# Kernel tuning notes

Measured on AMD Instinct MI355X. Metric: run time of the kernel, lower is better.

## Reference

```python
import jax, jax.numpy as jnp
import numpy as np

N_NODES = 65536
N_EDGES = 524288
GRAPH_SIZE = 512  # equal-size graphs -> batch = arange(N)//512
N_GRAPHS = N_NODES // GRAPH_SIZE
IN_DIM, HID, OUT_DIM, HEADS = 64, 64, 128, 4


def setup_inputs() -> dict:
    key = jax.random.key(0)
    ks = jax.random.split(key, 24)
    s = 0.1  # init scale
    # within-graph random edges
    g = jax.random.randint(ks[0], (N_EDGES,), 0, N_GRAPHS)
    off = jax.random.randint(ks[1], (2, N_EDGES), 0, GRAPH_SIZE)
    edge_index = (g[None, :] * GRAPH_SIZE + off).astype(jnp.int32)
    batch = (jnp.arange(N_NODES) // GRAPH_SIZE).astype(jnp.int32)
    rn = lambda k, sh: jax.random.normal(k, sh, jnp.float32) * s
    return {
        'x': jax.random.normal(ks[2], (N_NODES, IN_DIM), jnp.float32),
        'edge_index': edge_index, 'batch': batch,
        'W1': rn(ks[3], (IN_DIM, HEADS * HID)), 'a1s': rn(ks[4], (HEADS, HID)),
        'a1d': rn(ks[5], (HEADS, HID)), 'b1': jnp.zeros((HEADS * HID,), jnp.float32),
        'W2': rn(ks[6], (HEADS * HID, HEADS * HID)), 'a2s': rn(ks[7], (HEADS, HID)),
        'a2d': rn(ks[8], (HEADS, HID)), 'b2': jnp.zeros((HEADS * HID,), jnp.float32),
        'W3': rn(ks[9], (HEADS * HID, OUT_DIM)), 'a3s': rn(ks[10], (1, OUT_DIM)),
        'a3d': rn(ks[11], (1, OUT_DIM)), 'b3': jnp.zeros((OUT_DIM,), jnp.float32),
        'g1': jnp.ones((HEADS * HID,), jnp.float32), 'be1': jnp.zeros((HEADS * HID,), jnp.float32),
        'g2': jnp.ones((HEADS * HID,), jnp.float32), 'be2': jnp.zeros((HEADS * HID,), jnp.float32),
        'Wr': rn(ks[12], (IN_DIM, OUT_DIM)), 'br': jnp.zeros((OUT_DIM,), jnp.float32),
        'Wq': rn(ks[13], (OUT_DIM, OUT_DIM)), 'Wk': rn(ks[14], (OUT_DIM, OUT_DIM)),
        'Wv': rn(ks[15], (OUT_DIM, OUT_DIM)), 'Wo': rn(ks[16], (OUT_DIM, OUT_DIM)),
        'bo': jnp.zeros((OUT_DIM,), jnp.float32),
    }


def _gat(x, src, dst, W, a_s, a_d, b, heads, out_ch):
    N = x.shape[0]
    h = (x @ W).reshape(N, heads, out_ch)          # [N,H,C]
    e_s = (h * a_s).sum(-1)                        # [N,H]
    e_d = (h * a_d).sum(-1)
    e = jax.nn.leaky_relu(e_s[src] + e_d[dst], 0.2)  # [E,H]
    m = jax.ops.segment_max(e, dst, num_segments=N)
    p = jnp.exp(e - m[dst])
    z = jax.ops.segment_sum(p, dst, num_segments=N)
    alpha = p / (z[dst] + 1e-16)
    out = jax.ops.segment_sum(alpha[:, :, None] * h[src], dst, num_segments=N)
    return out.reshape(N, heads * out_ch) + b


def _ln(x, g, b):
    mu = x.mean(-1, keepdims=True)
    v = ((x - mu) ** 2).mean(-1, keepdims=True)
    return (x - mu) * jax.lax.rsqrt(v + 1e-5) * g + b


def _mha(x, Wq, Wk, Wv, Wo, bo, heads):
    B, n, D = x.shape
    hd = D // heads
    q = (x @ Wq).reshape(B, n, heads, hd)
    k = (x @ Wk).reshape(B, n, heads, hd)
    v = (x @ Wv).reshape(B, n, heads, hd)
    energy = jnp.einsum('bqhd,bkhd->bhqk', q, k)
    att = jax.nn.softmax(energy / jnp.sqrt(jnp.float32(D)), axis=-1)
    out = jnp.einsum('bhqk,bkhd->bqhd', att, v).reshape(B, n, D)
    return out @ Wo + bo


def reference(x, edge_index, batch, W1, a1s, a1d, b1, W2, a2s, a2d, b2,
              W3, a3s, a3d, b3, g1, be1, g2, be2, Wr, br, Wq, Wk, Wv, Wo, bo):
    N = x.shape[0]
    loops = jnp.arange(N, dtype=edge_index.dtype)
    src = jnp.concatenate([edge_index[0], loops])  # PyG add_self_loops default
    dst = jnp.concatenate([edge_index[1], loops])
    h = jax.nn.elu(_gat(x, src, dst, W1, a1s, a1d, b1, HEADS, HID))
    h = _ln(h, g1, be1)
    h = jax.nn.elu(_gat(h, src, dst, W2, a2s, a2d, b2, HEADS, HID))
    h = _ln(h, g2, be2)
    h = _gat(h, src, dst, W3, a3s, a3d, b3, 1, OUT_DIM)
    h = h + (x @ Wr + br)
    # equal-size graphs: per-graph self-attention via batched reshape
    hg = h.reshape(N_GRAPHS, GRAPH_SIZE, OUT_DIM)
    hg = _mha(hg, Wq, Wk, Wv, Wo, bo, 4)
    return hg.reshape(N, OUT_DIM)
```

## Files before the change

### kernel.cpp

```cpp
#include <hip/hip_runtime.h>
#include <math.h>

#define N_NODES 65536
#define NUM_EDGES 524288
#define E_TOT   (NUM_EDGES + N_NODES)
#define GSZ 512

typedef _Float16 f16x8 __attribute__((ext_vector_type(8)));
typedef _Float16 f16x4 __attribute__((ext_vector_type(4)));
typedef _Float16 f16x2 __attribute__((ext_vector_type(2)));
typedef float    f32x16 __attribute__((ext_vector_type(16)));

__global__ void k_zero_int(int* __restrict__ p, int n) {
  int i = blockIdx.x * blockDim.x + threadIdx.x;
  if (i < n) p[i] = 0;
}

__global__ void k_hist(const int* __restrict__ ei, int* __restrict__ cnt) {
  int e = blockIdx.x * blockDim.x + threadIdx.x;
  if (e >= E_TOT) return;
  int dst = (e < NUM_EDGES) ? ei[NUM_EDGES + e] : (e - NUM_EDGES);
  atomicAdd(&cnt[dst], 1);
}

__global__ void k_scan1(const int* __restrict__ cnt, int* __restrict__ offs,
                        int* __restrict__ sums) {
  __shared__ int s[256];
  int t = threadIdx.x;
  int i = blockIdx.x * 256 + t;
  int v = cnt[i];
  s[t] = v;
  for (int o = 1; o < 256; o <<= 1) {
    __syncthreads();
    int x = (t >= o) ? s[t - o] : 0;
    __syncthreads();
    s[t] += x;
  }
  offs[i] = s[t] - v;
  if (t == 255) sums[blockIdx.x] = s[t];
}

__global__ void k_scan2(int* __restrict__ sums) {
  __shared__ int s[256];
  int t = threadIdx.x;
  int v = sums[t];
  s[t] = v;
  for (int o = 1; o < 256; o <<= 1) {
    __syncthreads();
    int x = (t >= o) ? s[t - o] : 0;
    __syncthreads();
    s[t] += x;
  }
  sums[t] = s[t] - v;
}

__global__ void k_scan3(int* __restrict__ offs, const int* __restrict__ sums,
                        int* __restrict__ cur) {
  int i = blockIdx.x * 256 + threadIdx.x;
  int v = offs[i] + sums[blockIdx.x];
  offs[i] = v;
  cur[i] = v;
  if (i == 0) offs[N_NODES] = E_TOT;
}

__global__ void k_fill(const int* __restrict__ ei, int* __restrict__ cur,
                       int* __restrict__ ssrc) {
  int e = blockIdx.x * blockDim.x + threadIdx.x;
  if (e >= E_TOT) return;
  int src, dst;
  if (e < NUM_EDGES) { src = ei[e]; dst = ei[NUM_EDGES + e]; }
  else               { src = e - NUM_EDGES; dst = src; }
  int pos = atomicAdd(&cur[dst], 1);
  ssrc[pos] = src;
}

__device__ __forceinline__ f16x8 cvt8(float4 a, float4 b) {
  f16x8 h;
  h[0] = (_Float16)a.x; h[1] = (_Float16)a.y;
  h[2] = (_Float16)a.z; h[3] = (_Float16)a.w;
  h[4] = (_Float16)b.x; h[5] = (_Float16)b.y;
  h[6] = (_Float16)b.z; h[7] = (_Float16)b.w;
  return h;
}

#define LDH 40
template <typename TA, typename TC>
__global__ __launch_bounds__(256) void k_gemm(
    const TA* __restrict__ A, const float* __restrict__ B,
    const float* __restrict__ bias, TC* __restrict__ C,
    int M, int N, int K, float cscale) {
  __shared__ __align__(16) _Float16 As[128][LDH];
  __shared__ __align__(16) _Float16 Bs[128][LDH];
  const int t = threadIdx.x;
  const int l = t & 63, w = t >> 6;
  const int m0 = blockIdx.x * 128, n0 = blockIdx.y * 128;
  const int wm = (w >> 1) * 64, wn = (w & 1) * 64;
  const int lm = l & 31, kq = l >> 5;

  f32x16 acc00 = {}, acc01 = {}, acc10 = {}, acc11 = {};

  const int ra = t >> 1, ka = (t & 1) << 4;
  const int nb = (t & 31) << 2, kb = (t >> 5) << 2;

  for (int k0 = 0; k0 < K; k0 += 32) {
    f16x8 a_lo, a_hi;
    if constexpr (sizeof(TA) == 4) {
      const float* ap = (const float*)&A[(size_t)(m0 + ra) * K + k0 + ka];
      float4 av0 = *(const float4*)ap;
      float4 av1 = *(const float4*)(ap + 4);
      float4 av2 = *(const float4*)(ap + 8);
      float4 av3 = *(const float4*)(ap + 12);
      a_lo = cvt8(av0, av1);
      a_hi = cvt8(av2, av3);
    } else {
      const _Float16* ap = (const _Float16*)&A[(size_t)(m0 + ra) * K + k0 + ka];
      a_lo = *(const f16x8*)ap;
      a_hi = *(const f16x8*)(ap + 8);
    }
    const float* bp = &B[(size_t)(k0 + kb) * N + n0 + nb];
    float4 bv0 = *(const float4*)bp;
    float4 bv1 = *(const float4*)(bp + N);
    float4 bv2 = *(const float4*)(bp + 2 * N);
    float4 bv3 = *(const float4*)(bp + 3 * N);
    __syncthreads();
    *(f16x8*)&As[ra][ka]     = a_lo;
    *(f16x8*)&As[ra][ka + 8] = a_hi;
    f16x4 g;
    g[0] = (_Float16)bv0.x; g[1] = (_Float16)bv1.x;
    g[2] = (_Float16)bv2.x; g[3] = (_Float16)bv3.x;
    *(f16x4*)&Bs[nb + 0][kb] = g;
    g[0] = (_Float16)bv0.y; g[1] = (_Float16)bv1.y;
    g[2] = (_Float16)bv2.y; g[3] = (_Float16)bv3.y;
    *(f16x4*)&Bs[nb + 1][kb] = g;
    g[0] = (_Float16)bv0.z; g[1] = (_Float16)bv1.z;
    g[2] = (_Float16)bv2.z; g[3] = (_Float16)bv3.z;
    *(f16x4*)&Bs[nb + 2][kb] = g;
    g[0] = (_Float16)bv0.w; g[1] = (_Float16)bv1.w;
    g[2] = (_Float16)bv2.w; g[3] = (_Float16)bv3.w;
    *(f16x4*)&Bs[nb + 3][kb] = g;
    __syncthreads();
#pragma unroll
    for (int ks = 0; ks < 2; ++ks) {
      f16x8 a0 = *(const f16x8*)&As[wm + lm][ks * 16 + kq * 8];
      f16x8 a1 = *(const f16x8*)&As[wm + 32 + lm][ks * 16 + kq * 8];
      f16x8 b0 = *(const f16x8*)&Bs[wn + lm][ks * 16 + kq * 8];
      f16x8 b1 = *(const f16x8*)&Bs[wn + 32 + lm][ks * 16 + kq * 8];
      acc00 = __builtin_amdgcn_mfma_f32_32x32x16_f16(a0, b0, acc00, 0, 0, 0);
      acc01 = __builtin_amdgcn_mfma_f32_32x32x16_f16(a0, b1, acc01, 0, 0, 0);
      acc10 = __builtin_amdgcn_mfma_f32_32x32x16_f16(a1, b0, acc10, 0, 0, 0);
      acc11 = __builtin_amdgcn_mfma_f32_32x32x16_f16(a1, b1, acc11, 0, 0, 0);
    }
  }

  const int cn = n0 + wn + lm;
  float b0v = 0.f, b1v = 0.f;
  if (bias) { b0v = bias[cn]; b1v = bias[cn + 32]; }
  const int rb = 4 * (l >> 5);
#pragma unroll
  for (int r = 0; r < 16; ++r) {
    int row = m0 + wm + (r & 3) + 8 * (r >> 2) + rb;
    C[(size_t)row * N + cn]             = (TC)((acc00[r] + b0v) * cscale);
    C[(size_t)row * N + cn + 32]        = (TC)((acc01[r] + b1v) * cscale);
    C[(size_t)(row + 32) * N + cn]      = (TC)((acc10[r] + b0v) * cscale);
    C[(size_t)(row + 32) * N + cn + 32] = (TC)((acc11[r] + b1v) * cscale);
  }
}

__global__ void k_scores(const _Float16* __restrict__ h, const float* __restrict__ as_,
                         const float* __restrict__ ad_, float* __restrict__ es,
                         float* __restrict__ ed, int H, int C) {
  int t = blockIdx.x * blockDim.x + threadIdx.x;
  if (t >= N_NODES * H) return;
  int hd = t % H;
  const _Float16* hp = h + (size_t)t * C;
  const float* ap = as_ + hd * C;
  const float* dp = ad_ + hd * C;
  float s = 0.f, d = 0.f;
  for (int c = 0; c < C; c += 8) {
    f16x8 hv = *(const f16x8*)&hp[c];
    float4 a0 = *(const float4*)&ap[c];
    float4 a1 = *(const float4*)&ap[c + 4];
    float4 d0 = *(const float4*)&dp[c];
    float4 d1 = *(const float4*)&dp[c + 4];
    float h0 = (float)hv[0], h1 = (float)hv[1], h2 = (float)hv[2], h3 = (float)hv[3];
    float h4 = (float)hv[4], h5 = (float)hv[5], h6 = (float)hv[6], h7 = (float)hv[7];
    s += h0 * a0.x + h1 * a0.y + h2 * a0.z + h3 * a0.w;
    s += h4 * a1.x + h5 * a1.y + h6 * a1.z + h7 * a1.w;
    d += h0 * d0.x + h1 * d0.y + h2 * d0.z + h3 * d0.w;
    d += h4 * d1.x + h5 * d1.y + h6 * d1.z + h7 * d1.w;
  }
  es[t] = s; ed[t] = d;
}

__device__ __forceinline__ float lrelu02(float e) { return e >= 0.f ? e : 0.2f * e; }

__global__ __launch_bounds__(256) void k_agg256(
    const _Float16* __restrict__ h, const float* __restrict__ es,
    const float* __restrict__ ed, const int* __restrict__ offs,
    const int* __restrict__ ssrc, const float* __restrict__ bias,
    const float* __restrict__ lng, const float* __restrict__ lnb,
    _Float16* __restrict__ out) {
  int lane = threadIdx.x & 63;
  int bid = blockIdx.x;
  int swz = (bid & 7) * ((int)gridDim.x >> 3) + (bid >> 3);
  int n = swz * 4 + (threadIdx.x >> 6);
  int head = lane >> 4;
  int o0 = offs[n], deg = offs[n + 1] - o0;
  float4 edv = *(const float4*)&ed[n * 4];
  float edh = (head & 2) ? ((head & 1) ? edv.w : edv.z)
                         : ((head & 1) ? edv.y : edv.x);
  float z = 0.f, a0 = 0.f, a1 = 0.f, a2 = 0.f, a3 = 0.f;
  int c0 = lane * 4;
  int j = 0;
  for (; j + 2 <= deg; j += 2) {
    int s0 = ssrc[o0 + j], s1 = ssrc[o0 + j + 1];
    float p0 = __expf(fminf(lrelu02(es[s0 * 4 + head] + edh), 80.f));
    float p1 = __expf(fminf(lrelu02(es[s1 * 4 + head] + edh), 80.f));
    f16x4 h0 = *(const f16x4*)&h[(size_t)s0 * 256 + c0];
    f16x4 h1 = *(const f16x4*)&h[(size_t)s1 * 256 + c0];
    z += p0 + p1;
    a0 += p0 * (float)h0[0] + p1 * (float)h1[0];
    a1 += p0 * (float)h0[1] + p1 * (float)h1[1];
    a2 += p0 * (float)h0[2] + p1 * (float)h1[2];
    a3 += p0 * (float)h0[3] + p1 * (float)h1[3];
  }
  if (j < deg) {
    int s0 = ssrc[o0 + j];
    float p0 = __expf(fminf(lrelu02(es[s0 * 4 + head] + edh), 80.f));
    f16x4 h0 = *(const f16x4*)&h[(size_t)s0 * 256 + c0];
    z += p0;
    a0 += p0 * (float)h0[0]; a1 += p0 * (float)h0[1];
    a2 += p0 * (float)h0[2]; a3 += p0 * (float)h0[3];
  }
  float inv = 1.f / (z + 1e-16f);
  float4 bv = *(const float4*)&bias[c0];
  float v0 = a0 * inv + bv.x; v0 = v0 > 0.f ? v0 : __expf(v0) - 1.f;
  float v1 = a1 * inv + bv.y; v1 = v1 > 0.f ? v1 : __expf(v1) - 1.f;
  float v2 = a2 * inv + bv.z; v2 = v2 > 0.f ? v2 : __expf(v2) - 1.f;
  float v3 = a3 * inv + bv.w; v3 = v3 > 0.f ? v3 : __expf(v3) - 1.f;
  float sum = v0 + v1 + v2 + v3;
#pragma unroll
  for (int o = 1; o < 64; o <<= 1) sum += __shfl_xor(sum, o);
  float mean = sum * (1.f / 256.f);
  float d0 = v0 - mean, d1 = v1 - mean, d2 = v2 - mean, d3 = v3 - mean;
  float sq = d0 * d0 + d1 * d1 + d2 * d2 + d3 * d3;
#pragma unroll
  for (int o = 1; o < 64; o <<= 1) sq += __shfl_xor(sq, o);
  float rs = rsqrtf(sq * (1.f / 256.f) + 1e-5f);
  float4 gv = *(const float4*)&lng[c0];
  float4 ev2 = *(const float4*)&lnb[c0];
  f16x4 o4;
  o4[0] = (_Float16)(d0 * rs * gv.x + ev2.x);
  o4[1] = (_Float16)(d1 * rs * gv.y + ev2.y);
  o4[2] = (_Float16)(d2 * rs * gv.z + ev2.z);
  o4[3] = (_Float16)(d3 * rs * gv.w + ev2.w);
  *(f16x4*)&out[(size_t)n * 256 + c0] = o4;
}

__global__ __launch_bounds__(256) void k_agg128(
    const _Float16* __restrict__ h, const float* __restrict__ es,
    const float* __restrict__ ed, const int* __restrict__ offs,
    const int* __restrict__ ssrc, const float* __restrict__ bias,
    float* __restrict__ io) {
  int lane = threadIdx.x & 63;
  int bid = blockIdx.x;
  int swz = (bid & 7) * ((int)gridDim.x >> 3) + (bid >> 3);
  int n = swz * 4 + (threadIdx.x >> 6);
  int o0 = offs[n], deg = offs[n + 1] - o0;
  float edv = ed[n];
  float z = 0.f, a0 = 0.f, a1 = 0.f;
  int c0 = lane * 2;
  int j = 0;
  for (; j + 2 <= deg; j += 2) {
    int s0 = ssrc[o0 + j], s1 = ssrc[o0 + j + 1];
    float p0 = __expf(fminf(lrelu02(es[s0] + edv), 80.f));
    float p1 = __expf(fminf(lrelu02(es[s1] + edv), 80.f));
    f16x2 h0 = *(const f16x2*)&h[(size_t)s0 * 128 + c0];
    f16x2 h1 = *(const f16x2*)&h[(size_t)s1 * 128 + c0];
    z += p0 + p1;
    a0 += p0 * (float)h0[0] + p1 * (float)h1[0];
    a1 += p0 * (float)h0[1] + p1 * (float)h1[1];
  }
  if (j < deg) {
    int s0 = ssrc[o0 + j];
    float p0 = __expf(fminf(lrelu02(es[s0] + edv), 80.f));
    f16x2 h0 = *(const f16x2*)&h[(size_t)s0 * 128 + c0];
    z += p0;
    a0 += p0 * (float)h0[0]; a1 += p0 * (float)h0[1];
  }
  float inv = 1.f / (z + 1e-16f);
  float2 r = *(const float2*)&io[(size_t)n * 128 + c0];
  float2 o2;
  o2.x = a0 * inv + bias[c0]     + r.x;
  o2.y = a1 * inv + bias[c0 + 1] + r.y;
  *(float2*)&io[(size_t)n * 128 + c0] = o2;
}

__global__ __launch_bounds__(512) void k_attn(
    const _Float16* __restrict__ Q, const _Float16* __restrict__ K,
    const _Float16* __restrict__ V, _Float16* __restrict__ O) {
  __shared__ __align__(16) _Float16 Ks[64][40];
  __shared__ __align__(16) _Float16 VsT[32][72];
  const int g = blockIdx.x >> 2, hd = blockIdx.x & 3;
  const int t = threadIdx.x;
  const int l = t & 63, w = t >> 6;
  const int h = l >> 5, l31 = l & 31;
  const size_t base = (size_t)g * (GSZ * 128) + hd * 32;

  f16x8 qf[2][2];
#pragma unroll
  for (int j = 0; j < 2; ++j)
#pragma unroll
    for (int ks = 0; ks < 2; ++ks)
      qf[j][ks] = *(const f16x8*)&Q[base + (size_t)(w * 64 + j * 32 + l31) * 128 + ks * 16 + 8 * h];

  f32x16 o0 = {}, o1 = {};
  float la0 = 0.f, la1 = 0.f, m0 = -1e30f, m1 = -1e30f;

  const int kr = t >> 3, dc = (t & 7) * 4;
  for (int kt = 0; kt < GSZ; kt += 64) {
    f16x4 kg = *(const f16x4*)&K[base + (size_t)(kt + kr) * 128 + dc];
    f16x4 vg = *(const f16x4*)&V[base + (size_t)(kt + kr) * 128 + dc];
    __syncthreads();
    *(f16x4*)&Ks[kr][dc] = kg;
    VsT[dc + 0][kr] = vg[0];
    VsT[dc + 1][kr] = vg[1];
    VsT[dc + 2][kr] = vg[2];
    VsT[dc + 3][kr] = vg[3];
    __syncthreads();

#pragma unroll
    for (int s2 = 0; s2 < 2; ++s2) {
      f16x8 ka0 = *(const f16x8*)&Ks[s2 * 32 + l31][8 * h];
      f16x8 ka1 = *(const f16x8*)&Ks[s2 * 32 + l31][16 + 8 * h];
      f16x8 va0 = *(const f16x8*)&VsT[l31][s2 * 32 + 8 * h];
      f16x8 va1 = *(const f16x8*)&VsT[l31][s2 * 32 + 16 + 8 * h];
#pragma unroll
      for (int j = 0; j < 2; ++j) {
        f32x16 s = {};
        s = __builtin_amdgcn_mfma_f32_32x32x16_f16(ka0, qf[j][0], s, 0, 0, 0);
        s = __builtin_amdgcn_mfma_f32_32x32x16_f16(ka1, qf[j][1], s, 0, 0, 0);
        float tm = s[0];
#pragma unroll
        for (int r = 1; r < 16; ++r) tm = fmaxf(tm, s[r]);
        tm = fmaxf(tm, __shfl_xor(tm, 32));
        float* mj = j ? &m1 : &m0;
        float* lj = j ? &la1 : &la0;
        f32x16* oj = j ? &o1 : &o0;
        if (tm > *mj + 10.f) {
          float sc = exp2f(*mj - tm);
          *lj *= sc;
#pragma unroll
          for (int r = 0; r < 16; ++r) (*oj)[r] *= sc;
          *mj = tm;
        }
        float p[16]; float ls = 0.f;
#pragma unroll
        for (int r = 0; r < 16; ++r) { p[r] = exp2f(s[r] - *mj); ls += p[r]; }
        *lj += ls;
#pragma unroll
        for (int kk = 0; kk < 2; ++kk) {
          const int rb = kk * 8;
          unsigned a01 = __builtin_bit_cast(unsigned, __builtin_amdgcn_cvt_pkrtz(p[rb + 0], p[rb + 1]));
          unsigned a23 = __builtin_bit_cast(unsigned, __builtin_amdgcn_cvt_pkrtz(p[rb + 2], p[rb + 3]));
          unsigned b01 = __builtin_bit_cast(unsigned, __builtin_amdgcn_cvt_pkrtz(p[rb + 4], p[rb + 5]));
          unsigned b23 = __builtin_bit_cast(unsigned, __builtin_amdgcn_cvt_pkrtz(p[rb + 6], p[rb + 7]));
          unsigned sa01 = (unsigned)__shfl_xor((int)a01, 32);
          unsigned sa23 = (unsigned)__shfl_xor((int)a23, 32);
          unsigned sb01 = (unsigned)__shfl_xor((int)b01, 32);
          unsigned sb23 = (unsigned)__shfl_xor((int)b23, 32);
          union { unsigned u[4]; f16x8 v; } pb;
          pb.u[0] = h ? sb01 : a01;
          pb.u[1] = h ? sb23 : a23;
          pb.u[2] = h ? b01 : sa01;
          pb.u[3] = h ? b23 : sa23;
          *oj = __builtin_amdgcn_mfma_f32_32x32x16_f16(kk ? va1 : va0, pb.v, *oj, 0, 0, 0);
        }
      }
    }
  }

  la0 += __shfl_xor(la0, 32);
  la1 += __shfl_xor(la1, 32);
  const float i0 = 1.f / la0, i1 = 1.f / la1;
#pragma unroll
  for (int r = 0; r < 16; ++r) {
    int dv = (r & 3) + 8 * (r >> 2) + 4 * h;
    O[base + (size_t)(w * 64 + l31) * 128 + dv]      = (_Float16)(o0[r] * i0);
    O[base + (size_t)(w * 64 + 32 + l31) * 128 + dv] = (_Float16)(o1[r] * i1);
  }
}

extern "C" void kernel_launch(void* const* d_in, const int* in_sizes, int n_in,
                              void* d_out, int out_size, void* d_ws, size_t ws_size,
                              hipStream_t stream) {
  (void)in_sizes; (void)n_in; (void)out_size; (void)ws_size;
  const float* x   = (const float*)d_in[0];
  const int*   ei  = (const int*)d_in[1];
  const float* W1  = (const float*)d_in[3];
  const float* a1s = (const float*)d_in[4];
  const float* a1d = (const float*)d_in[5];
  const float* b1  = (const float*)d_in[6];
  const float* W2  = (const float*)d_in[7];
  const float* a2s = (const float*)d_in[8];
  const float* a2d = (const float*)d_in[9];
  const float* b2  = (const float*)d_in[10];
  const float* W3  = (const float*)d_in[11];
  const float* a3s = (const float*)d_in[12];
  const float* a3d = (const float*)d_in[13];
  const float* b3  = (const float*)d_in[14];
  const float* g1  = (const float*)d_in[15];
  const float* be1 = (const float*)d_in[16];
  const float* g2  = (const float*)d_in[17];
  const float* be2 = (const float*)d_in[18];
  const float* Wr  = (const float*)d_in[19];
  const float* br  = (const float*)d_in[20];
  const float* Wq  = (const float*)d_in[21];
  const float* Wk  = (const float*)d_in[22];
  const float* Wv  = (const float*)d_in[23];
  const float* Wo  = (const float*)d_in[24];
  const float* bo  = (const float*)d_in[25];
  float* out = (float*)d_out;

  _Float16* Hbuf = (_Float16*)d_ws;
  _Float16* Abuf = Hbuf + (size_t)N_NODES * 256;
  float* esb = (float*)(Abuf + (size_t)N_NODES * 256);
  float* edb = esb + (size_t)N_NODES * 4;
  int* offs = (int*)(edb + (size_t)N_NODES * 4);
  int* cur  = offs + N_NODES + 4;
  int* ssrc = cur + N_NODES;
  int* sums = ssrc + E_TOT;

  dim3 blk(256), blk512(512);
  k_zero_int<<<256, blk, 0, stream>>>(cur, N_NODES);
  k_hist<<<(E_TOT + 255) / 256, blk, 0, stream>>>(ei, cur);
  k_scan1<<<256, blk, 0, stream>>>(cur, offs, sums);
  k_scan2<<<1, blk, 0, stream>>>(sums);
  k_scan3<<<256, blk, 0, stream>>>(offs, sums, cur);
  k_fill<<<(E_TOT + 255) / 256, blk, 0, stream>>>(ei, cur, ssrc);

  dim3 gN128(512, 1), gN256(512, 2);
  const float qsc = 0.0883883476483184f * 1.44269504088896f;

  k_gemm<float, float><<<gN128, blk, 0, stream>>>(x, Wr, br, out, N_NODES, 128, 64, 1.f);

  k_gemm<float, _Float16><<<gN256, blk, 0, stream>>>(x, W1, nullptr, Hbuf, N_NODES, 256, 64, 1.f);
  k_scores<<<N_NODES * 4 / 256, blk, 0, stream>>>(Hbuf, a1s, a1d, esb, edb, 4, 64);
  k_agg256<<<N_NODES / 4, blk, 0, stream>>>(Hbuf, esb, edb, offs, ssrc, b1, g1, be1, Abuf);
  k_gemm<_Float16, _Float16><<<gN256, blk, 0, stream>>>(Abuf, W2, nullptr, Hbuf, N_NODES, 256, 256, 1.f);
  k_scores<<<N_NODES * 4 / 256, blk, 0, stream>>>(Hbuf, a2s, a2d, esb, edb, 4, 64);
  k_agg256<<<N_NODES / 4, blk, 0, stream>>>(Hbuf, esb, edb, offs, ssrc, b2, g2, be2, Abuf);
  k_gemm<_Float16, _Float16><<<gN128, blk, 0, stream>>>(Abuf, W3, nullptr, Hbuf, N_NODES, 128, 256, 1.f);
  k_scores<<<N_NODES / 256, blk, 0, stream>>>(Hbuf, a3s, a3d, esb, edb, 1, 128);
  k_agg128<<<N_NODES / 4, blk, 0, stream>>>(Hbuf, esb, edb, offs, ssrc, b3, out);

  _Float16* Qb  = Abuf;
  _Float16* Kb  = Abuf + (size_t)N_NODES * 128;
  _Float16* Vb  = Hbuf;
  _Float16* AOb = Hbuf + (size_t)N_NODES * 128;
  k_gemm<float, _Float16><<<gN128, blk, 0, stream>>>(out, Wq, nullptr, Qb, N_NODES, 128, 128, qsc);
  k_gemm<float, _Float16><<<gN128, blk, 0, stream>>>(out, Wk, nullptr, Kb, N_NODES, 128, 128, 1.f);
  k_gemm<float, _Float16><<<gN128, blk, 0, stream>>>(out, Wv, nullptr, Vb, N_NODES, 128, 128, 1.f);
  k_attn<<<512, blk512, 0, stream>>>(Qb, Kb, Vb, AOb);
  k_gemm<_Float16, float><<<gN128, blk, 0, stream>>>(AOb, Wo, bo, out, N_NODES, 128, 128, 1.f);
}
```

Before: 534.9 us.

## Fuse QKV projections into one GEMM and double-buffer attention K/V tiles

Concatenates Wq, Wk and Wv into one 128x384 weight matrix so a single GEMM produces Q, K and V in an interleaved buffer, with the softmax scale applied only to the Q column block. This reads the activation input once instead of three times and saves two launches. The attention kernel now uses 256-thread blocks, each covering half of a graph's queries, and double-buffers the K/V shared-memory tiles so the next tile's global load overlaps the MFMA work. The trade-off is a small weight-concat kernel on every call, strided 384-wide reads of K/V, and K/V tiles loaded twice per head (once per query half).

```diff
diff --git a/kernel.cpp b/kernel.cpp
--- a/kernel.cpp
+++ b/kernel.cpp
@@ -74,6 +74,17 @@
   ssrc[pos] = src;
 }
 
+__global__ void k_catw(const float* __restrict__ Wq, const float* __restrict__ Wk,
+                       const float* __restrict__ Wv, float* __restrict__ Wcat) {
+  int i = blockIdx.x * 256 + threadIdx.x;
+  if (i >= 128 * 384) return;
+  int k = i / 384, j = i - k * 384;
+  float v = (j < 128) ? Wq[k * 128 + j]
+          : (j < 256) ? Wk[k * 128 + j - 128]
+                      : Wv[k * 128 + j - 256];
+  Wcat[i] = v;
+}
+
 __device__ __forceinline__ f16x8 cvt8(float4 a, float4 b) {
   f16x8 h;
   h[0] = (_Float16)a.x; h[1] = (_Float16)a.y;
@@ -88,7 +99,7 @@
 __global__ __launch_bounds__(256) void k_gemm(
     const TA* __restrict__ A, const float* __restrict__ B,
     const float* __restrict__ bias, TC* __restrict__ C,
-    int M, int N, int K, float cscale) {
+    int M, int N, int K, float cscale, int sy) {
   __shared__ __align__(16) _Float16 As[128][LDH];
   __shared__ __align__(16) _Float16 Bs[128][LDH];
   const int t = threadIdx.x;
@@ -96,6 +107,7 @@
   const int m0 = blockIdx.x * 128, n0 = blockIdx.y * 128;
   const int wm = (w >> 1) * 64, wn = (w & 1) * 64;
   const int lm = l & 31, kq = l >> 5;
+  const float cs = (blockIdx.y == sy) ? cscale : 1.f;
 
   f32x16 acc00 = {}, acc01 = {}, acc10 = {}, acc11 = {};
 
@@ -159,10 +171,10 @@
 #pragma unroll
   for (int r = 0; r < 16; ++r) {
     int row = m0 + wm + (r & 3) + 8 * (r >> 2) + rb;
-    C[(size_t)row * N + cn]             = (TC)((acc00[r] + b0v) * cscale);
-    C[(size_t)row * N + cn + 32]        = (TC)((acc01[r] + b1v) * cscale);
-    C[(size_t)(row + 32) * N + cn]      = (TC)((acc10[r] + b0v) * cscale);
-    C[(size_t)(row + 32) * N + cn + 32] = (TC)((acc11[r] + b1v) * cscale);
+    C[(size_t)row * N + cn]             = (TC)((acc00[r] + b0v) * cs);
+    C[(size_t)row * N + cn + 32]        = (TC)((acc01[r] + b1v) * cs);
+    C[(size_t)(row + 32) * N + cn]      = (TC)((acc10[r] + b0v) * cs);
+    C[(size_t)(row + 32) * N + cn + 32] = (TC)((acc11[r] + b1v) * cs);
   }
 }
 
@@ -296,53 +308,65 @@
   *(float2*)&io[(size_t)n * 128 + c0] = o2;
 }
 
-__global__ __launch_bounds__(512) void k_attn(
-    const _Float16* __restrict__ Q, const _Float16* __restrict__ K,
-    const _Float16* __restrict__ V, _Float16* __restrict__ O) {
-  __shared__ __align__(16) _Float16 Ks[64][40];
-  __shared__ __align__(16) _Float16 VsT[32][72];
-  const int g = blockIdx.x >> 2, hd = blockIdx.x & 3;
+__global__ __launch_bounds__(256) void k_attn(
+    const _Float16* __restrict__ QKV, _Float16* __restrict__ O) {
+  __shared__ __align__(16) _Float16 Ks[2][64][40];
+  __shared__ __align__(16) _Float16 VsT[2][32][72];
+  const int bid = blockIdx.x;
+  const int g = bid >> 3, hd = (bid >> 1) & 3, qh = bid & 1;
   const int t = threadIdx.x;
   const int l = t & 63, w = t >> 6;
   const int h = l >> 5, l31 = l & 31;
-  const size_t base = (size_t)g * (GSZ * 128) + hd * 32;
+  const size_t nbase = (size_t)g * GSZ;
+  const _Float16* Qp = QKV + hd * 32;
+  const _Float16* Kp = QKV + 128 + hd * 32;
+  const _Float16* Vp = QKV + 256 + hd * 32;
 
   f16x8 qf[2][2];
 #pragma unroll
   for (int j = 0; j < 2; ++j)
 #pragma unroll
     for (int ks = 0; ks < 2; ++ks)
-      qf[j][ks] = *(const f16x8*)&Q[base + (size_t)(w * 64 + j * 32 + l31) * 128 + ks * 16 + 8 * h];
+      qf[j][ks] = *(const f16x8*)&Qp[(nbase + qh * 256 + w * 64 + j * 32 + l31) * 384 + ks * 16 + 8 * h];
 
   f32x16 o0 = {}, o1 = {};
   float la0 = 0.f, la1 = 0.f, m0 = -1e30f, m1 = -1e30f;
 
-  const int kr = t >> 3, dc = (t & 7) * 4;
+  const int kr = t >> 2, dcc = (t & 3) * 8;
+  {
+    f16x8 kg = *(const f16x8*)&Kp[(nbase + kr) * 384 + dcc];
+    f16x8 vg = *(const f16x8*)&Vp[(nbase + kr) * 384 + dcc];
+    *(f16x8*)&Ks[0][kr][dcc] = kg;
+#pragma unroll
+    for (int i = 0; i < 8; ++i) VsT[0][dcc + i][kr] = vg[i];
+  }
+  __syncthreads();
+
   for (int kt = 0; kt < GSZ; kt += 64) {
-    f16x4 kg = *(const f16x4*)&K[base + (size_t)(kt + kr) * 128 + dc];
-    f16x4 vg = *(const f16x4*)&V[base + (size_t)(kt + kr) * 128 + dc];
-    __syncthreads();
-    *(f16x4*)&Ks[kr][dc] = kg;
-    VsT[dc + 0][kr] = vg[0];
-    VsT[dc + 1][kr] = vg[1];
-    VsT[dc + 2][kr] = vg[2];
-    VsT[dc + 3][kr] = vg[3];
-    __syncthreads();
-
+    const int cur = (kt >> 6) & 1;
+    const bool more = (kt + 64) < GSZ;
+    f16x8 kn, vn;
+    if (more) {
+      kn = *(const f16x8*)&Kp[(nbase + kt + 64 + kr) * 384 + dcc];
+      vn = *(const f16x8*)&Vp[(nbase + kt + 64 + kr) * 384 + dcc];
+    }
 #pragma unroll
     for (int s2 = 0; s2 < 2; ++s2) {
-      f16x8 ka0 = *(const f16x8*)&Ks[s2 * 32 + l31][8 * h];
-      f16x8 ka1 = *(const f16x8*)&Ks[s2 * 32 + l31][16 + 8 * h];
-      f16x8 va0 = *(const f16x8*)&VsT[l31][s2 * 32 + 8 * h];
-      f16x8 va1 = *(const f16x8*)&VsT[l31][s2 * 32 + 16 + 8 * h];
+      f16x8 ka0 = *(const f16x8*)&Ks[cur][s2 * 32 + l31][8 * h];
+      f16x8 ka1 = *(const f16x8*)&Ks[cur][s2 * 32 + l31][16 + 8 * h];
+      f16x8 va0 = *(const f16x8*)&VsT[cur][l31][s2 * 32 + 8 * h];
+      f16x8 va1 = *(const f16x8*)&VsT[cur][l31][s2 * 32 + 16 + 8 * h];
 #pragma unroll
       for (int j = 0; j < 2; ++j) {
         f32x16 s = {};
         s = __builtin_amdgcn_mfma_f32_32x32x16_f16(ka0, qf[j][0], s, 0, 0, 0);
         s = __builtin_amdgcn_mfma_f32_32x32x16_f16(ka1, qf[j][1], s, 0, 0, 0);
-        float tm = s[0];
-#pragma unroll
-        for (int r = 1; r < 16; ++r) tm = fmaxf(tm, s[r]);
+        float t0 = fmaxf(fmaxf(s[0], s[1]), s[2]);
+        float t1 = fmaxf(fmaxf(s[3], s[4]), s[5]);
+        float t2 = fmaxf(fmaxf(s[6], s[7]), s[8]);
+        float t3 = fmaxf(fmaxf(s[9], s[10]), s[11]);
+        float t4 = fmaxf(fmaxf(s[12], s[13]), s[14]);
+        float tm = fmaxf(fmaxf(fmaxf(t0, t1), fmaxf(t2, t3)), fmaxf(t4, s[15]));
         tm = fmaxf(tm, __shfl_xor(tm, 32));
         float* mj = j ? &m1 : &m0;
         float* lj = j ? &la1 : &la0;
@@ -378,6 +402,12 @@
         }
       }
     }
+    if (more) {
+      *(f16x8*)&Ks[cur ^ 1][kr][dcc] = kn;
+#pragma unroll
+      for (int i = 0; i < 8; ++i) VsT[cur ^ 1][dcc + i][kr] = vn[i];
+    }
+    __syncthreads();
   }
 
   la0 += __shfl_xor(la0, 32);
@@ -386,8 +416,8 @@
 #pragma unroll
   for (int r = 0; r < 16; ++r) {
     int dv = (r & 3) + 8 * (r >> 2) + 4 * h;
-    O[base + (size_t)(w * 64 + l31) * 128 + dv]      = (_Float16)(o0[r] * i0);
-    O[base + (size_t)(w * 64 + 32 + l31) * 128 + dv] = (_Float16)(o1[r] * i1);
+    O[(nbase + qh * 256 + w * 64 + l31) * 128 + hd * 32 + dv]      = (_Float16)(o0[r] * i0);
+    O[(nbase + qh * 256 + w * 64 + 32 + l31) * 128 + hd * 32 + dv] = (_Float16)(o1[r] * i1);
   }
 }
 
@@ -424,43 +454,41 @@
 
   _Float16* Hbuf = (_Float16*)d_ws;
   _Float16* Abuf = Hbuf + (size_t)N_NODES * 256;
-  float* esb = (float*)(Abuf + (size_t)N_NODES * 256);
+  _Float16* QKVb = Abuf + (size_t)N_NODES * 256;
+  _Float16* AOb  = QKVb + (size_t)N_NODES * 384;
+  float* esb = (float*)(AOb + (size_t)N_NODES * 128);
   float* edb = esb + (size_t)N_NODES * 4;
-  int* offs = (int*)(edb + (size_t)N_NODES * 4);
+  float* Wcat = edb + (size_t)N_NODES * 4;
+  int* offs = (int*)(Wcat + 128 * 384);
   int* cur  = offs + N_NODES + 4;
   int* ssrc = cur + N_NODES;
   int* sums = ssrc + E_TOT;
 
-  dim3 blk(256), blk512(512);
+  dim3 blk(256);
   k_zero_int<<<256, blk, 0, stream>>>(cur, N_NODES);
   k_hist<<<(E_TOT + 255) / 256, blk, 0, stream>>>(ei, cur);
   k_scan1<<<256, blk, 0, stream>>>(cur, offs, sums);
   k_scan2<<<1, blk, 0, stream>>>(sums);
   k_scan3<<<256, blk, 0, stream>>>(offs, sums, cur);
   k_fill<<<(E_TOT + 255) / 256, blk, 0, stream>>>(ei, cur, ssrc);
-
-  dim3 gN128(512, 1), gN256(512, 2);
+  k_catw<<<192, blk, 0, stream>>>(Wq, Wk, Wv, Wcat);
+
+  dim3 gN128(512, 1), gN256(512, 2), gN384(512, 3);
   const float qsc = 0.0883883476483184f * 1.44269504088896f;
 
-  k_gemm<float, float><<<gN128, blk, 0, stream>>>(x, Wr, br, out, N_NODES, 128, 64, 1.f);
-
-  k_gemm<float, _Float16><<<gN256, blk, 0, stream>>>(x, W1, nullptr, Hbuf, N_NODES, 256, 64, 1.f);
+  k_gemm<float, float><<<gN128, blk, 0, stream>>>(x, Wr, br, out, N_NODES, 128, 64, 1.f, -1);
+
+  k_gemm<float, _Float16><<<gN256, blk, 0, stream>>>(x, W1, nullptr, Hbuf, N_NODES, 256, 64, 1.f, -1);
   k_scores<<<N_NODES * 4 / 256, blk, 0, stream>>>(Hbuf, a1s, a1d, esb, edb, 4, 64);
   k_agg256<<<N_NODES / 4, blk, 0, stream>>>(Hbuf, esb, edb, offs, ssrc, b1, g1, be1, Abuf);
-  k_gemm<_Float16, _Float16><<<gN256, blk, 0, stream>>>(Abuf, W2, nullptr, Hbuf, N_NODES, 256, 256, 1.f);
+  k_gemm<_Float16, _Float16><<<gN256, blk, 0, stream>>>(Abuf, W2, nullptr, Hbuf, N_NODES, 256, 256, 1.f, -1);
   k_scores<<<N_NODES * 4 / 256, blk, 0, stream>>>(Hbuf, a2s, a2d, esb, edb, 4, 64);
   k_agg256<<<N_NODES / 4, blk, 0, stream>>>(Hbuf, esb, edb, offs, ssrc, b2, g2, be2, Abuf);
-  k_gemm<_Float16, _Float16><<<gN128, blk, 0, stream>>>(Abuf, W3, nullptr, Hbuf, N_NODES, 128, 256, 1.f);
+  k_gemm<_Float16, _Float16><<<gN128, blk, 0, stream>>>(Abuf, W3, nullptr, Hbuf, N_NODES, 128, 256, 1.f, -1);
   k_scores<<<N_NODES / 256, blk, 0, stream>>>(Hbuf, a3s, a3d, esb, edb, 1, 128);
   k_agg128<<<N_NODES / 4, blk, 0, stream>>>(Hbuf, esb, edb, offs, ssrc, b3, out);
 
-  _Float16* Qb  = Abuf;
-  _Float16* Kb  = Abuf + (size_t)N_NODES * 128;
-  _Float16* Vb  = Hbuf;
-  _Float16* AOb = Hbuf + (size_t)N_NODES * 128;
-  k_gemm<float, _Float16><<<gN128, blk, 0, stream>>>(out, Wq, nullptr, Qb, N_NODES, 128, 128, qsc);
-  k_gemm<float, _Float16><<<gN128, blk, 0, stream>>>(out, Wk, nullptr, Kb, N_NODES, 128, 128, 1.f);
-  k_gemm<float, _Float16><<<gN128, blk, 0, stream>>>(out, Wv, nullptr, Vb, N_NODES, 128, 128, 1.f);
-  k_attn<<<512, blk512, 0, stream>>>(Qb, Kb, Vb, AOb);
-  k_gemm<_Float16, float><<<gN128, blk, 0, stream>>>(AOb, Wo, bo, out, N_NODES, 128, 128, 1.f);
-}
+  k_gemm<float, _Float16><<<gN384, blk, 0, stream>>>(out, Wcat, nullptr, QKVb, N_NODES, 384, 128, qsc, 0);
+  k_attn<<<1024, blk, 0, stream>>>(QKVb, AOb);
+  k_gemm<_Float16, float><<<gN128, blk, 0, stream>>>(AOb, Wo, bo, out, N_NODES, 128, 128, 1.f, -1);
+}
```

Result: no change. 534.5 us (-0.1%).
